# Performance work log

Measured on AMD Instinct MI355X. Metric: run time of the kernel, lower is better.

The kernel has to match this reference:

```python
import jax, jax.numpy as jnp
import numpy as np

N = 1
IN_C = 256
NUM_ANCHORS = 9
NUM_CLASSES = 91
# (H, W, stride) per FPN level for an 800x800 input
LEVELS = [(100, 100, 8), (50, 50, 16), (25, 25, 32), (13, 13, 64), (7, 7, 128)]
BBOX_CLAMP = float(np.log(1000.0 / 16.0))


def setup_inputs() -> dict:
    key = jax.random.key(0)
    ks = jax.random.split(key, 12)
    std = 0.01
    inp = {}
    for i, (h, w, _) in enumerate(LEVELS):
        inp[f"feat{i}"] = jax.random.normal(ks[i], (N, IN_C, h, w), jnp.float32)
    inp["cls_tw"] = jax.random.normal(ks[5], (4, IN_C, IN_C, 3, 3), jnp.float32) * std
    inp["cls_tb"] = jnp.zeros((4, IN_C), jnp.float32)
    inp["cls_out_w"] = jax.random.normal(ks[6], (NUM_ANCHORS * NUM_CLASSES, IN_C, 3, 3), jnp.float32) * std
    # prior-probability bias init: -log((1-p)/p) with p=0.01
    inp["cls_out_b"] = jnp.full((NUM_ANCHORS * NUM_CLASSES,), -np.log((1 - 0.01) / 0.01), jnp.float32)
    inp["reg_tw"] = jax.random.normal(ks[7], (4, IN_C, IN_C, 3, 3), jnp.float32) * std
    inp["reg_tb"] = jnp.zeros((4, IN_C), jnp.float32)
    inp["reg_out_w"] = jax.random.normal(ks[8], (NUM_ANCHORS * 4, IN_C, 3, 3), jnp.float32) * std
    inp["reg_out_b"] = jnp.zeros((NUM_ANCHORS * 4,), jnp.float32)
    return inp


def _conv3(x, w, b):
    y = jax.lax.conv_general_dilated(x, w, (1, 1), [(1, 1), (1, 1)],
                                     dimension_numbers=("NCHW", "OIHW", "NCHW"))
    return y + b[None, :, None, None]


def _run_head(feat, tw, tb, ow, ob, K):
    x = feat
    for i in range(4):  # fixed 4-layer tower
        x = jax.nn.relu(_conv3(x, tw[i], tb[i]))
    y = _conv3(x, ow, ob)                      # [N, A*K, H, W]
    n, _, h, w = y.shape
    y = y.reshape(n, -1, K, h, w)              # [N, A, K, H, W]
    y = jnp.transpose(y, (0, 3, 4, 1, 2))      # [N, H, W, A, K]
    return y.reshape(n, -1, K)                 # [N, H*W*A, K]


def _make_anchors():
    base_sizes = [32.0, 64.0, 128.0, 256.0, 512.0]
    scales = np.array([2 ** (i / 3.0) for i in range(3)], np.float32)
    ratios = np.array([0.5, 1.0, 2.0], np.float32)
    h_ratios = np.sqrt(ratios)
    w_ratios = 1.0 / h_ratios
    out = []
    for lvl, (H, W, stride) in enumerate(LEVELS):
        sizes = base_sizes[lvl] * scales                      # [3]
        ws = (w_ratios[:, None] * sizes[None, :]).reshape(-1)  # [9], ratio-major
        hs = (h_ratios[:, None] * sizes[None, :]).reshape(-1)
        base = np.stack([-ws, -hs, ws, hs], axis=1) / 2.0      # [9, 4]
        sy = np.arange(H, dtype=np.float32) * stride
        sx = np.arange(W, dtype=np.float32) * stride
        yy, xx = np.meshgrid(sy, sx, indexing="ij")
        shifts = np.stack([xx, yy, xx, yy], axis=-1).reshape(-1, 4)  # [H*W, 4]
        out.append((shifts[:, None, :] + base[None, :, :]).reshape(-1, 4))
    return jnp.asarray(np.concatenate(out, axis=0))  # [A_total, 4]


def _decode(reg, anchors):
    # torchvision BoxCoder.decode with weights (1,1,1,1)
    aw = anchors[:, 2] - anchors[:, 0]
    ah = anchors[:, 3] - anchors[:, 1]
    acx = anchors[:, 0] + 0.5 * aw
    acy = anchors[:, 1] + 0.5 * ah
    dx, dy, dw, dh = reg[..., 0], reg[..., 1], reg[..., 2], reg[..., 3]
    dw = jnp.minimum(dw, BBOX_CLAMP)
    dh = jnp.minimum(dh, BBOX_CLAMP)
    pcx = dx * aw + acx
    pcy = dy * ah + acy
    pw = jnp.exp(dw) * aw
    ph = jnp.exp(dh) * ah
    return jnp.stack([pcx - 0.5 * pw, pcy - 0.5 * ph, pcx + 0.5 * pw, pcy + 0.5 * ph], axis=-1)


def reference(feat0, feat1, feat2, feat3, feat4,
              cls_tw, cls_tb, cls_out_w, cls_out_b,
              reg_tw, reg_tb, reg_out_w, reg_out_b):
    feats = [feat0, feat1, feat2, feat3, feat4]
    cls_logits = jnp.concatenate(
        [_run_head(f, cls_tw, cls_tb, cls_out_w, cls_out_b, NUM_CLASSES) for f in feats], axis=1)
    bbox_reg = jnp.concatenate(
        [_run_head(f, reg_tw, reg_tb, reg_out_w, reg_out_b, 4) for f in feats], axis=1)
    anchors = _make_anchors()                     # [A_total, 4]
    boxes = _decode(bbox_reg, anchors)            # [N, A_total, 4]
    scores = jax.nn.sigmoid(cls_logits)           # [N, A_total, 91]
    return jnp.concatenate([scores, boxes], axis=-1)  # [N, A_total, 95]
```

## Files before the change

kernel.cpp:

```cpp
#include <hip/hip_runtime.h>
#include <math.h>

typedef unsigned short u16;
typedef __attribute__((ext_vector_type(8))) short s8v;
typedef __attribute__((ext_vector_type(4))) float f4v;

#define NUM_CLASSES 91
#define NUM_ANCHORS 9
#define NT2 247
#define TG8 31
#define TW_STRIDE (256*256*9)
#define PSTRIDE 872

struct Tab {
    int tstart[5];
    int tw[5];
    int H[5], W[5], GP0[5];
};

__device__ __forceinline__ u16 f2bf(float f) {
    unsigned u = __float_as_uint(f);
    u += 0x7fffu + ((u >> 16) & 1u);
    return (u16)(u >> 16);
}

__device__ __forceinline__ void pack_one(const float* __restrict__ w,
                                         u16* __restrict__ dst,
                                         int idx, int c_out_real)
{
    int lane = idx & 63;
    int t2 = idx >> 6;
    int chunk = t2 % 72;
    int co16 = t2 / 72;
    int tap = chunk >> 3, cib = chunk & 7;
    int co = co16 * 16 + (lane & 15);
    int ci0 = cib * 32 + ((lane >> 4) << 3);
    s8v v8;
    #pragma unroll
    for (int j = 0; j < 8; ++j) {
        float v = (co < c_out_real) ? w[((co << 8) + ci0 + j) * 9 + tap] : 0.f;
        v8[j] = (short)f2bf(v);
    }
    *(s8v*)(dst + (size_t)idx * 8) = v8;
}

#define PACK_TOTAL (8 * 72 * 16 * 64 + 72 * 52 * 64 + 72 * 3 * 64)
#define PACK_BLKS  ((PACK_TOTAL + 255) / 256)
#define CONV_BLKS  ((13343 + 63) / 64)

__global__ __launch_bounds__(256) void prep_all(
    const float* __restrict__ cls_tw, const float* __restrict__ reg_tw,
    const float* __restrict__ cls_ow, const float* __restrict__ reg_ow,
    u16* __restrict__ pt, size_t pt_stride_u16,
    u16* __restrict__ pc, u16* __restrict__ pr,
    const float* __restrict__ f0, const float* __restrict__ f1,
    const float* __restrict__ f2, const float* __restrict__ f3,
    const float* __restrict__ f4, u16* __restrict__ act, Tab tab)
{
    const int bid = blockIdx.x;
    if (bid < PACK_BLKS) {
        int idx = bid * 256 + threadIdx.x;
        const int per_t = 72 * 16 * 64;
        const int cls_n = 72 * 52 * 64;
        if (idx < 8 * per_t) {
            int layer = idx / per_t;
            int r = idx - layer * per_t;
            const float* src = (layer < 4) ? cls_tw + (size_t)layer * TW_STRIDE
                                           : reg_tw + (size_t)(layer - 4) * TW_STRIDE;
            pack_one(src, pt + (size_t)layer * pt_stride_u16, r, 256);
        } else if (idx < 8 * per_t + cls_n) {
            pack_one(cls_ow, pc, idx - 8 * per_t, 819);
        } else if (idx < PACK_TOTAL) {
            pack_one(reg_ow, pr, idx - 8 * per_t - cls_n, 36);
        }
    } else {
        int gp = (bid - PACK_BLKS) * 64 + (threadIdx.x & 63);
        int cg = threadIdx.x >> 6;
        if (gp >= 13343) return;
        int lvl = 0;
        if (gp >= tab.GP0[1]) lvl = 1;
        if (gp >= tab.GP0[2]) lvl = 2;
        if (gp >= tab.GP0[3]) lvl = 3;
        if (gp >= tab.GP0[4]) lvl = 4;
        const float* x = lvl == 0 ? f0 : lvl == 1 ? f1 : lvl == 2 ? f2
                       : lvl == 3 ? f3 : f4;
        int p = gp - tab.GP0[lvl];
        int HW = tab.H[lvl] * tab.W[lvl];
        #pragma unroll
        for (int pass = 0; pass < 8; ++pass) {
            int c0 = pass * 32 + cg * 8;
            s8v v8;
            #pragma unroll
            for (int j = 0; j < 8; ++j)
                v8[j] = (short)f2bf(x[(c0 + j) * HW + p]);
            *(s8v*)(act + (((size_t)gp << 8) + c0)) = v8;
        }
    }
}

__global__ __launch_bounds__(256) void pack_w(const float* __restrict__ w,
                                              u16* __restrict__ dst,
                                              int c_out_real, int nco16)
{
    int idx = blockIdx.x * 256 + threadIdx.x;
    if (idx < 72 * nco16 * 64) pack_one(w, dst, idx, c_out_real);
}

__global__ __launch_bounds__(256) void conv2bf_all(
    const float* __restrict__ f0, const float* __restrict__ f1,
    const float* __restrict__ f2, const float* __restrict__ f3,
    const float* __restrict__ f4, u16* __restrict__ out, Tab tab)
{
    int gp = blockIdx.x * 64 + (threadIdx.x & 63);
    int cg = threadIdx.x >> 6;
    if (gp >= 13343) return;
    int lvl = 0;
    if (gp >= tab.GP0[1]) lvl = 1;
    if (gp >= tab.GP0[2]) lvl = 2;
    if (gp >= tab.GP0[3]) lvl = 3;
    if (gp >= tab.GP0[4]) lvl = 4;
    const float* x = lvl == 0 ? f0 : lvl == 1 ? f1 : lvl == 2 ? f2 : lvl == 3 ? f3 : f4;
    int p = gp - tab.GP0[lvl];
    int HW = tab.H[lvl] * tab.W[lvl];
    #pragma unroll
    for (int pass = 0; pass < 8; ++pass) {
        int c0 = pass * 32 + cg * 8;
        s8v v8;
        #pragma unroll
        for (int j = 0; j < 8; ++j)
            v8[j] = (short)f2bf(x[(c0 + j) * HW + p]);
        *(s8v*)(out + (((size_t)gp << 8) + c0)) = v8;
    }
}

template<int MODE, int NCO16, int ACCN, int NTHR>
__device__ __forceinline__ void conv_core(
    u16* __restrict__ lds,
    const u16* __restrict__ act, const u16* __restrict__ wpk,
    const float* __restrict__ bias,
    u16* __restrict__ outw, float* __restrict__ fout,
    int bx, int by, const Tab& tab)
{
    constexpr int NW = NTHR / 64;
    constexpr int SJOBS = (864 + NTHR - 1) / NTHR;

    int lvl = 0;
    if (by >= tab.tstart[1]) lvl = 1;
    if (by >= tab.tstart[2]) lvl = 2;
    if (by >= tab.tstart[3]) lvl = 3;
    if (by >= tab.tstart[4]) lvl = 4;
    const int H = tab.H[lvl], W = tab.W[lvl], gp0 = tab.GP0[lvl];
    const int t = by - tab.tstart[lvl];
    const int tw = tab.tw[lvl];
    const int w0 = (t % tw) * 16;
    const int h0 = (t / tw) * 4;

    const int tid = threadIdx.x;
    const int lane = tid & 63, wv = tid >> 6;
    const int co16w = bx * (NW * ACCN) + wv * ACCN;
    const int kg = lane >> 4;
    const int col = lane & 15;

    int sofs[SJOBS], slds[SJOBS];
    bool svalid[SJOBS], slive[SJOBS];
    #pragma unroll
    for (int i = 0; i < SJOBS; ++i) {
        int k = tid + i * NTHR;
        slive[i] = k < 864;
        int kk = slive[i] ? k : 0;
        int px = kk >> 3, part = kk & 7;
        int hh = px / 18, ww = px - hh * 18;
        int gh = h0 + hh - 1, gw = w0 + ww - 1;
        svalid[i] = ((unsigned)gh < (unsigned)H) && ((unsigned)gw < (unsigned)W);
        sofs[i] = ((gp0 + gh * W + gw) << 8) + part * 8;
        slds[i] = part * PSTRIDE + px * 8;
    }

    const u16* bbn[ACCN];
    #pragma unroll
    for (int n = 0; n < ACCN; ++n) {
        int c = co16w + n;
        if (c >= NCO16) c = NCO16 - 1;
        bbn[n] = wpk + ((size_t)(c * 72) << 9) + (lane << 3);
    }

    f4v acc[4][ACCN];
    #pragma unroll
    for (int s = 0; s < 4; ++s)
        #pragma unroll
        for (int n = 0; n < ACCN; ++n)
            acc[s][n] = (f4v){0.f, 0.f, 0.f, 0.f};

    s8v pre[SJOBS];
    auto ISSUE_S = [&](int cc) {
        #pragma unroll
        for (int i = 0; i < SJOBS; ++i) {
            s8v v = {};
            if (slive[i] && svalid[i])
                v = *(const s8v*)(act + sofs[i] + cc * 64);
            pre[i] = v;
        }
    };

    ISSUE_S(0);
    #pragma unroll 1
    for (int cib = 0; cib < 4; ++cib) {
        if (cib) __syncthreads();
        #pragma unroll
        for (int i = 0; i < SJOBS; ++i)
            if (slive[i]) *(s8v*)(&lds[slds[i]]) = pre[i];
        __syncthreads();

        #pragma unroll
        for (int cs = 0; cs < 2; ++cs) {
            const u16* L = &lds[(cs * 4 + kg) * PSTRIDE];
            #pragma unroll
            for (int kx = 0; kx < 3; ++kx) {
                s8v a[6];
                #pragma unroll
                for (int r = 0; r < 6; ++r)
                    a[r] = *(const s8v*)(&L[(r * 18 + col + kx) * 8]);
                #pragma unroll
                for (int ky = 0; ky < 3; ++ky) {
                    s8v b[ACCN];
                    #pragma unroll
                    for (int n = 0; n < ACCN; ++n)
                        b[n] = *(const s8v*)(bbn[n] +
                            ((size_t)((ky * 3 + kx) * 8 + cib * 2 + cs) << 9));
                    #pragma unroll
                    for (int s = 0; s < 4; ++s)
                        #pragma unroll
                        for (int n = 0; n < ACCN; ++n)
                            acc[s][n] = __builtin_amdgcn_mfma_f32_16x16x32_bf16(
                                a[s + ky], b[n], acc[s][n], 0, 0, 0);
                }
                if (cs == 0 && kx == 0 && cib < 3) ISSUE_S(cib + 1);
            }
        }
    }

    #pragma unroll
    for (int n = 0; n < ACCN; ++n) {
        const int co = (co16w + n) * 16 + (lane & 15);
        if (co < NCO16 * 16) {
            #pragma unroll
            for (int s = 0; s < 4; ++s) {
                const int h = h0 + s;
                #pragma unroll
                for (int j = 0; j < 4; ++j) {
                    const int w = w0 + ((lane >> 4) << 2) + j;
                    if (h < H && w < W) {
                        const int p = h * W + w;
                        if (MODE == 0) {
                            float v = acc[s][n][j] + bias[co];
                            outw[((size_t)(gp0 + p) << 8) + co] = f2bf(fmaxf(v, 0.f));
                        } else if (MODE == 1) {
                            if (co < NUM_ANCHORS * NUM_CLASSES) {
                                float v = acc[s][n][j] + bias[co];
                                int a = co / NUM_CLASSES;
                                int k = co - a * NUM_CLASSES;
                                float sg = 1.f / (1.f + __expf(-v));
                                fout[((size_t)(gp0 + p) * 9 + a) * 95 + k] = sg;
                            }
                        } else {
                            if (co < 36)
                                fout[(gp0 + p) * 48 + co] = acc[s][n][j] + bias[co];
                        }
                    }
                }
            }
        }
    }
}


__global__ __launch_bounds__(512, 4) void conv_tower(
    const u16* __restrict__ actC, u16* __restrict__ outC,
    const u16* __restrict__ actR, u16* __restrict__ outR,
    const u16* __restrict__ wC, const u16* __restrict__ wR,
    const float* __restrict__ bC, const float* __restrict__ bR, Tab tab)
{
    __shared__ u16 lds[8 * PSTRIDE];
    const int s = blockIdx.x;
    const int xcd = s & 7;
    const int q = s >> 3;
    const int head = q & 1;
    const int t = (q >> 1) * 8 + xcd;
    if (t >= NT2) return;
    conv_core<0, 16, 2, 512>(lds, head ? actR : actC, head ? wR : wC,
                             head ? bR : bC, head ? outR : outC, nullptr,
                             0, t, tab);
}

__global__ __launch_bounds__(512, 4) void conv_cls(
    const u16* __restrict__ actD, const u16* __restrict__ wPC,
    const float* __restrict__ cls_ob, float* __restrict__ out, Tab tab)
{
    __shared__ u16 lds[8 * PSTRIDE];
    const int s = blockIdx.x;
    const int xcd = s & 7;
    const int q = s >> 3;
    const int pass = q & 3;
    const int t = (q >> 2) * 8 + xcd;
    if (t >= NT2) return;
    conv_core<1, 52, 2, 512>(lds, actD, wPC, cls_ob, nullptr, out, pass, t, tab);
}

__global__ __launch_bounds__(256, 4) void conv_reg(
    const u16* __restrict__ actA, const u16* __restrict__ wPR,
    const float* __restrict__ reg_ob, float* __restrict__ raw, Tab tab)
{
    __shared__ u16 lds[8 * PSTRIDE];
    conv_core<2, 3, 1, 256>(lds, actA, wPR, reg_ob, nullptr, raw,
                            0, blockIdx.x, tab);
}

__global__ __launch_bounds__(256) void decode_boxes(
    const float* __restrict__ raw, float* __restrict__ out, Tab tab)
{
    int idx = blockIdx.x * 256 + threadIdx.x;
    if (idx >= 13343 * 9) return;
    int gp = idx / 9, a = idx % 9;
    int lvl = 0;
    if (gp >= tab.GP0[1]) lvl = 1;
    if (gp >= tab.GP0[2]) lvl = 2;
    if (gp >= tab.GP0[3]) lvl = 3;
    if (gp >= tab.GP0[4]) lvl = 4;
    int p = gp - tab.GP0[lvl];
    int W = tab.W[lvl];
    int h = p / W, wc = p % W;
    float stride = (float)(8 << lvl);
    float base = (float)(32 << lvl);

    float dx = raw[gp * 48 + a * 4 + 0];
    float dy = raw[gp * 48 + a * 4 + 1];
    float dw = raw[gp * 48 + a * 4 + 2];
    float dh = raw[gp * 48 + a * 4 + 3];

    const float scales[3] = {1.f, 1.2599210498948732f, 1.5874010519681994f};
    const float hr[3] = {0.70710678118654752f, 1.f, 1.41421356237309505f};
    int ri = a / 3, si = a % 3;
    float sz = base * scales[si];
    float ah = hr[ri] * sz;
    float aw = sz / hr[ri];
    float acx = (float)wc * stride;
    float acy = (float)h * stride;

    const float CLAMP = 4.135166556742356f;
    dw = fminf(dw, CLAMP);
    dh = fminf(dh, CLAMP);
    float pcx = dx * aw + acx;
    float pcy = dy * ah + acy;
    float pw = expf(dw) * aw;
    float ph = expf(dh) * ah;

    float* o = out + ((size_t)gp * 9 + a) * 95 + 91;
    o[0] = pcx - 0.5f * pw;
    o[1] = pcy - 0.5f * ph;
    o[2] = pcx + 0.5f * pw;
    o[3] = pcy + 0.5f * ph;
}

extern "C" void kernel_launch(void* const* d_in, const int* in_sizes, int n_in,
                              void* d_out, int out_size, void* d_ws, size_t ws_size,
                              hipStream_t stream)
{
    const float* f0 = (const float*)d_in[0];
    const float* f1 = (const float*)d_in[1];
    const float* f2 = (const float*)d_in[2];
    const float* f3 = (const float*)d_in[3];
    const float* f4 = (const float*)d_in[4];
    const float* cls_tw = (const float*)d_in[5];
    const float* cls_tb = (const float*)d_in[6];
    const float* cls_ow = (const float*)d_in[7];
    const float* cls_ob = (const float*)d_in[8];
    const float* reg_tw = (const float*)d_in[9];
    const float* reg_tb = (const float*)d_in[10];
    const float* reg_ow = (const float*)d_in[11];
    const float* reg_ob = (const float*)d_in[12];
    float* out = (float*)d_out;

    static const Tab TAB = {
        {0, 175, 227, 241, 245},
        {7, 4, 2, 1, 1},
        {100, 50, 25, 13, 7},
        {100, 50, 25, 13, 7},
        {0, 10000, 12500, 13125, 13294}
    };

    char* wsb = (char*)d_ws;
    const size_t AS = 6832128;
    u16* A = (u16*)(wsb + 0 * AS);
    u16* B = (u16*)(wsb + 1 * AS);
    u16* C = (u16*)(wsb + 2 * AS);
    u16* D = (u16*)(wsb + 3 * AS);
    float* RAW = (float*)B;

    const u16* cin[4]   = {A, B, D, B};
    u16*       cout_[4] = {B, D, B, D};
    const u16* rin[4]   = {A, C, A, C};
    u16*       rout[4]  = {C, A, C, A};

    const size_t PTSZ = 1179648;
    const bool big = ws_size >= (4 * AS + 8 * PTSZ + 3833856 + 221184);

    const int GT = 8 * 2 * TG8;
    const int GC = 8 * 4 * TG8;

    if (big) {
        u16* PT = (u16*)(wsb + 4 * AS);
        u16* PC = (u16*)(wsb + 4 * AS + 8 * PTSZ);
        u16* PR = (u16*)(wsb + 4 * AS + 8 * PTSZ + 3833856);

        prep_all<<<PACK_BLKS + CONV_BLKS, 256, 0, stream>>>(
            cls_tw, reg_tw, cls_ow, reg_ow, PT, PTSZ / 2, PC, PR,
            f0, f1, f2, f3, f4, A, TAB);

        for (int s = 0; s < 4; ++s)
            conv_tower<<<GT, 512, 0, stream>>>(
                cin[s], cout_[s], rin[s], rout[s],
                PT + (size_t)s * (PTSZ / 2), PT + (size_t)(4 + s) * (PTSZ / 2),
                cls_tb + s * 256, reg_tb + s * 256, TAB);

        conv_cls<<<GC, 512, 0, stream>>>(D, PC, cls_ob, out, TAB);
        conv_reg<<<NT2, 256, 0, stream>>>(A, PR, reg_ob, RAW, TAB);
    } else {
        u16* PC = (u16*)(wsb + 4 * AS);
        u16* PR = (u16*)(wsb + 4 * AS + 3833856);
        conv2bf_all<<<CONV_BLKS, 256, 0, stream>>>(f0, f1, f2, f3, f4, A, TAB);
        for (int s = 0; s < 4; ++s) {
            pack_w<<<(72 * 16 * 64 + 255) / 256, 256, 0, stream>>>(cls_tw + s * TW_STRIDE, PC, 256, 16);
            pack_w<<<(72 * 16 * 64 + 255) / 256, 256, 0, stream>>>(reg_tw + s * TW_STRIDE, PR, 256, 16);
            conv_tower<<<GT, 512, 0, stream>>>(
                cin[s], cout_[s], rin[s], rout[s], PC, PR,
                cls_tb + s * 256, reg_tb + s * 256, TAB);
        }
        pack_w<<<(72 * 52 * 64 + 255) / 256, 256, 0, stream>>>(cls_ow, PC, 819, 52);
        conv_cls<<<GC, 512, 0, stream>>>(D, PC, cls_ob, out, TAB);
        pack_w<<<(72 * 3 * 64 + 255) / 256, 256, 0, stream>>>(reg_ow, PR, 36, 3);
        conv_reg<<<NT2, 256, 0, stream>>>(A, PR, reg_ob, RAW, TAB);
    }

    decode_boxes<<<(13343 * 9 + 255) / 256, 256, 0, stream>>>(RAW, out, TAB);
}
```

Before: 287.2 us.

## Merge cls and reg output convs into one launch with fused box decode

Replaces the separate classification-output conv, regression-output conv and decode_boxes kernels with one conv_out launch. Its grid covers both cls passes and reg tiles, and the reg branch decodes boxes in-kernel from an LDS staging buffer. This removes two launches, the raw-regression round trip through global memory, and lets the small reg conv overlap with the cls conv. The cost is that the reg path now runs with 512 threads instead of 256, and the fused decode adds LDS traffic and syncs at the end of those blocks.

After: 278.9 us (median of 2 runs). -2.9%, faster.

```diff
diff --git a/kernel.cpp b/kernel.cpp
--- a/kernel.cpp
+++ b/kernel.cpp
@@ -11,6 +11,7 @@
 #define TG8 31
 #define TW_STRIDE (256*256*9)
 #define PSTRIDE 872
+#define GC (8 * 4 * TG8)
 
 struct Tab {
     int tstart[5];
@@ -239,6 +240,56 @@
         }
     }
 
+    if (MODE == 2) {
+        float* Rf = (float*)lds;
+        __syncthreads();
+        #pragma unroll
+        for (int n = 0; n < ACCN; ++n) {
+            const int co = (co16w + n) * 16 + col;
+            if (co < 36) {
+                const float bval = bias[co];
+                #pragma unroll
+                for (int s = 0; s < 4; ++s)
+                    #pragma unroll
+                    for (int j = 0; j < 4; ++j) {
+                        int px = (s << 4) + ((lane >> 4) << 2) + j;
+                        Rf[px * 40 + co] = acc[s][n][j] + bval;
+                    }
+            }
+        }
+        __syncthreads();
+        const float stridef = (float)(8 << lvl);
+        const float basef = (float)(32 << lvl);
+        const float scales[3] = {1.f, 1.2599210498948732f, 1.5874010519681994f};
+        const float hrt[3] = {0.70710678118654752f, 1.f, 1.41421356237309505f};
+        const float CLAMP = 4.135166556742356f;
+        for (int job = tid; job < 576; job += NTHR) {
+            int px = job / 9, a = job - (job / 9) * 9;
+            int r = px >> 4, c = px & 15;
+            int gh = h0 + r, gw = w0 + c;
+            if (gh < H && gw < W) {
+                f4v d = *(const f4v*)(&Rf[px * 40 + a * 4]);
+                int ri = a / 3, si = a - ri * 3;
+                float sz = basef * scales[si];
+                float ah = hrt[ri] * sz;
+                float aw = sz / hrt[ri];
+                float acx = (float)gw * stridef;
+                float acy = (float)gh * stridef;
+                float dw = fminf(d[2], CLAMP);
+                float dh = fminf(d[3], CLAMP);
+                float pcx = d[0] * aw + acx;
+                float pcy = d[1] * ah + acy;
+                float pw = expf(dw) * aw;
+                float ph = expf(dh) * ah;
+                float* o = fout + ((size_t)(gp0 + gh * W + gw) * 9 + a) * 95 + 91;
+                o[0] = pcx - 0.5f * pw;
+                o[1] = pcy - 0.5f * ph;
+                o[2] = pcx + 0.5f * pw;
+                o[3] = pcy + 0.5f * ph;
+            }
+        }
+        return;
+    }
     #pragma unroll
     for (int n = 0; n < ACCN; ++n) {
         const int co = (co16w + n) * 16 + (lane & 15);
@@ -254,7 +305,7 @@
                         if (MODE == 0) {
                             float v = acc[s][n][j] + bias[co];
                             outw[((size_t)(gp0 + p) << 8) + co] = f2bf(fmaxf(v, 0.f));
-                        } else if (MODE == 1) {
+                        } else {
                             if (co < NUM_ANCHORS * NUM_CLASSES) {
                                 float v = acc[s][n][j] + bias[co];
                                 int a = co / NUM_CLASSES;
@@ -262,9 +313,6 @@
                                 float sg = 1.f / (1.f + __expf(-v));
                                 fout[((size_t)(gp0 + p) * 9 + a) * 95 + k] = sg;
                             }
-                        } else {
-                            if (co < 36)
-                                fout[(gp0 + p) * 48 + co] = acc[s][n][j] + bias[co];
                         }
                     }
                 }
@@ -292,73 +340,26 @@
                              0, t, tab);
 }
 
-__global__ __launch_bounds__(512, 4) void conv_cls(
-    const u16* __restrict__ actD, const u16* __restrict__ wPC,
-    const float* __restrict__ cls_ob, float* __restrict__ out, Tab tab)
+__global__ __launch_bounds__(512, 4) void conv_out(
+    const u16* __restrict__ actD, const u16* __restrict__ actA,
+    const u16* __restrict__ wPC, const u16* __restrict__ wPR,
+    const float* __restrict__ cls_ob, const float* __restrict__ reg_ob,
+    float* __restrict__ out, Tab tab)
 {
     __shared__ u16 lds[8 * PSTRIDE];
     const int s = blockIdx.x;
-    const int xcd = s & 7;
-    const int q = s >> 3;
-    const int pass = q & 3;
-    const int t = (q >> 2) * 8 + xcd;
-    if (t >= NT2) return;
-    conv_core<1, 52, 2, 512>(lds, actD, wPC, cls_ob, nullptr, out, pass, t, tab);
-}
-
-__global__ __launch_bounds__(256, 4) void conv_reg(
-    const u16* __restrict__ actA, const u16* __restrict__ wPR,
-    const float* __restrict__ reg_ob, float* __restrict__ raw, Tab tab)
-{
-    __shared__ u16 lds[8 * PSTRIDE];
-    conv_core<2, 3, 1, 256>(lds, actA, wPR, reg_ob, nullptr, raw,
-                            0, blockIdx.x, tab);
-}
-
-__global__ __launch_bounds__(256) void decode_boxes(
-    const float* __restrict__ raw, float* __restrict__ out, Tab tab)
-{
-    int idx = blockIdx.x * 256 + threadIdx.x;
-    if (idx >= 13343 * 9) return;
-    int gp = idx / 9, a = idx % 9;
-    int lvl = 0;
-    if (gp >= tab.GP0[1]) lvl = 1;
-    if (gp >= tab.GP0[2]) lvl = 2;
-    if (gp >= tab.GP0[3]) lvl = 3;
-    if (gp >= tab.GP0[4]) lvl = 4;
-    int p = gp - tab.GP0[lvl];
-    int W = tab.W[lvl];
-    int h = p / W, wc = p % W;
-    float stride = (float)(8 << lvl);
-    float base = (float)(32 << lvl);
-
-    float dx = raw[gp * 48 + a * 4 + 0];
-    float dy = raw[gp * 48 + a * 4 + 1];
-    float dw = raw[gp * 48 + a * 4 + 2];
-    float dh = raw[gp * 48 + a * 4 + 3];
-
-    const float scales[3] = {1.f, 1.2599210498948732f, 1.5874010519681994f};
-    const float hr[3] = {0.70710678118654752f, 1.f, 1.41421356237309505f};
-    int ri = a / 3, si = a % 3;
-    float sz = base * scales[si];
-    float ah = hr[ri] * sz;
-    float aw = sz / hr[ri];
-    float acx = (float)wc * stride;
-    float acy = (float)h * stride;
-
-    const float CLAMP = 4.135166556742356f;
-    dw = fminf(dw, CLAMP);
-    dh = fminf(dh, CLAMP);
-    float pcx = dx * aw + acx;
-    float pcy = dy * ah + acy;
-    float pw = expf(dw) * aw;
-    float ph = expf(dh) * ah;
-
-    float* o = out + ((size_t)gp * 9 + a) * 95 + 91;
-    o[0] = pcx - 0.5f * pw;
-    o[1] = pcy - 0.5f * ph;
-    o[2] = pcx + 0.5f * pw;
-    o[3] = pcy + 0.5f * ph;
+    if (s < GC) {
+        const int xcd = s & 7;
+        const int q = s >> 3;
+        const int pass = q & 3;
+        const int t = (q >> 2) * 8 + xcd;
+        if (t >= NT2) return;
+        conv_core<1, 52, 2, 512>(lds, actD, wPC, cls_ob, nullptr, out,
+                                 pass, t, tab);
+    } else {
+        conv_core<2, 3, 1, 512>(lds, actA, wPR, reg_ob, nullptr, out,
+                                0, s - GC, tab);
+    }
 }
 
 extern "C" void kernel_launch(void* const* d_in, const int* in_sizes, int n_in,
@@ -394,7 +395,6 @@
     u16* B = (u16*)(wsb + 1 * AS);
     u16* C = (u16*)(wsb + 2 * AS);
     u16* D = (u16*)(wsb + 3 * AS);
-    float* RAW = (float*)B;
 
     const u16* cin[4]   = {A, B, D, B};
     u16*       cout_[4] = {B, D, B, D};
@@ -405,7 +405,7 @@
     const bool big = ws_size >= (4 * AS + 8 * PTSZ + 3833856 + 221184);
 
     const int GT = 8 * 2 * TG8;
-    const int GC = 8 * 4 * TG8;
+    const int GO = GC + NT2;
 
     if (big) {
         u16* PT = (u16*)(wsb + 4 * AS);
@@ -422,8 +422,7 @@
                 PT + (size_t)s * (PTSZ / 2), PT + (size_t)(4 + s) * (PTSZ / 2),
                 cls_tb + s * 256, reg_tb + s * 256, TAB);
 
-        conv_cls<<<GC, 512, 0, stream>>>(D, PC, cls_ob, out, TAB);
-        conv_reg<<<NT2, 256, 0, stream>>>(A, PR, reg_ob, RAW, TAB);
+        conv_out<<<GO, 512, 0, stream>>>(D, A, PC, PR, cls_ob, reg_ob, out, TAB);
     } else {
         u16* PC = (u16*)(wsb + 4 * AS);
         u16* PR = (u16*)(wsb + 4 * AS + 3833856);
@@ -436,10 +435,7 @@
                 cls_tb + s * 256, reg_tb + s * 256, TAB);
         }
         pack_w<<<(72 * 52 * 64 + 255) / 256, 256, 0, stream>>>(cls_ow, PC, 819, 52);
-        conv_cls<<<GC, 512, 0, stream>>>(D, PC, cls_ob, out, TAB);
         pack_w<<<(72 * 3 * 64 + 255) / 256, 256, 0, stream>>>(reg_ow, PR, 36, 3);
-        conv_reg<<<NT2, 256, 0, stream>>>(A, PR, reg_ob, RAW, TAB);
-    }
-
-    decode_boxes<<<(13343 * 9 + 255) / 256, 256, 0, stream>>>(RAW, out, TAB);
-}
+        conv_out<<<GO, 512, 0, stream>>>(D, A, PC, PR, cls_ob, reg_ob, out, TAB);
+    }
+}
```
